# Performance work log

Hardware: AMD Instinct MI355X
Metric: run time of the kernel (lower is better)

Reference implementation:

```python
import jax, jax.numpy as jnp
import numpy as np

N_NODES = 50000
N_EDGES = 1600000
OUT_FEATURES = 32


def setup_inputs() -> dict:
    key = jax.random.key(0)
    k_edge, k_w = jax.random.split(key)
    edge = jax.random.randint(k_edge, (2, N_EDGES), 0, N_NODES, dtype=jnp.int64 if jax.config.jax_enable_x64 else jnp.int32)
    edge_w = jax.random.normal(k_w, (N_EDGES, OUT_FEATURES), dtype=jnp.float32)
    return {
        "edge": edge,
        "edge_w": edge_w,
        "num_nodes": N_NODES,
        "E": N_EDGES,
        "out_features": OUT_FEATURES,
    }


def reference(edge, edge_w, num_nodes, E, out_features):
    # torch: sparse_coo_tensor(edge, edge_w, [N, N, F]); torch.sparse.sum(dim=1).to_dense()
    # == segment-sum of edge_w over source indices edge[0] into N buckets.
    src = edge[0]  # (E,)
    out = jax.ops.segment_sum(edge_w, src, num_segments=num_nodes)  # (N, F)
    return out
```

## Files before the change

kernel.cpp:

```cpp
#include <hip/hip_runtime.h>


constexpr int F = 32;
constexpr int NPB = 64;
constexpr int CAP = 3072;
constexpr int SLOT = 97;
constexpr int TILE = 6272;
constexpr int TSLOT = 44;
constexpr int STH = 1024;
constexpr int ATH = 512;

__global__ void __launch_bounds__(1024) zero_cursor(int* __restrict__ cursor, int nbuck) {
  int t = threadIdx.x;
  if (t < nbuck) cursor[t] = 0;
}

__global__ void __launch_bounds__(STH) bucket_scatter(
    const int* __restrict__ src, int* __restrict__ cursor,
    int* __restrict__ blist, int E, int nbuck) {
  extern __shared__ int lds[];
  int* slots = lds;
  int* scnt  = lds + nbuck * TSLOT;
  int t0 = blockIdx.x * TILE;
  int mEnd = min(TILE, E - t0);
  if (mEnd <= 0) return;
  for (int i = threadIdx.x; i < nbuck; i += STH) scnt[i] = 0;
  __syncthreads();
  const int4* src4 = reinterpret_cast<const int4*>(src + t0);
  int m4 = mEnd >> 2;
  for (int j = threadIdx.x; j < m4; j += STH) {
    int4 v = src4[j];
    int e = t0 + (j << 2);
    int b0 = v.x >> 6, p0 = atomicAdd(&scnt[b0], 1);
    if (p0 < TSLOT) slots[b0 * TSLOT + p0] = ((v.x & 63) << 21) | e;
    int b1 = v.y >> 6, p1 = atomicAdd(&scnt[b1], 1);
    if (p1 < TSLOT) slots[b1 * TSLOT + p1] = ((v.y & 63) << 21) | (e + 1);
    int b2 = v.z >> 6, p2 = atomicAdd(&scnt[b2], 1);
    if (p2 < TSLOT) slots[b2 * TSLOT + p2] = ((v.z & 63) << 21) | (e + 2);
    int b3 = v.w >> 6, p3 = atomicAdd(&scnt[b3], 1);
    if (p3 < TSLOT) slots[b3 * TSLOT + p3] = ((v.w & 63) << 21) | (e + 3);
  }
  for (int j = (m4 << 2) + threadIdx.x; j < mEnd; j += STH) {
    int sv = src[t0 + j];
    int b = sv >> 6, p = atomicAdd(&scnt[b], 1);
    if (p < TSLOT) slots[b * TSLOT + p] = ((sv & 63) << 21) | (t0 + j);
  }
  __syncthreads();
  for (int b = threadIdx.x; b < nbuck; b += STH) {
    int c = min(scnt[b], TSLOT);
    if (c) {
      int gbase = b * CAP + atomicAdd(&cursor[b], c);
      const int* s = &slots[b * TSLOT];
      for (int j = 0; j < c; ++j) blist[gbase + j] = s[j];
    }
  }
}

__global__ void __launch_bounds__(ATH) bucket_accum(
    const int* __restrict__ blist, const int* __restrict__ cursor,
    const float* __restrict__ w, float* __restrict__ out, int N) {
  __shared__ int sorted[NPB * SLOT];
  __shared__ int cur[NPB];
  int b = blockIdx.x;
  int t = threadIdx.x;
  int g = t >> 3;
  int ln = t & 7;
  const float4* w4 = reinterpret_cast<const float4*>(w);

  if (t < NPB) cur[t] = 0;
  int beg = b * CAP;
  int cnt_b = cursor[b];
  __syncthreads();

  const int4* bl4 = reinterpret_cast<const int4*>(blist + beg);
  int m4 = cnt_b >> 2;
  for (int i = t; i < m4; i += ATH) {
    int4 v = bl4[i];
    int p0 = atomicAdd(&cur[v.x >> 21], 1);
    if (p0 < SLOT) sorted[(v.x >> 21) * SLOT + p0] = v.x & 0x1FFFFF;
    int p1 = atomicAdd(&cur[v.y >> 21], 1);
    if (p1 < SLOT) sorted[(v.y >> 21) * SLOT + p1] = v.y & 0x1FFFFF;
    int p2 = atomicAdd(&cur[v.z >> 21], 1);
    if (p2 < SLOT) sorted[(v.z >> 21) * SLOT + p2] = v.z & 0x1FFFFF;
    int p3 = atomicAdd(&cur[v.w >> 21], 1);
    if (p3 < SLOT) sorted[(v.w >> 21) * SLOT + p3] = v.w & 0x1FFFFF;
  }
  for (int i = (m4 << 2) + t; i < cnt_b; i += ATH) {
    int v = blist[beg + i];
    int node = v >> 21;
    int pos = atomicAdd(&cur[node], 1);
    if (pos < SLOT) sorted[node * SLOT + pos] = v & 0x1FFFFF;
  }
  __syncthreads();

  int ke = min(cur[g], SLOT);
  const int* myList = &sorted[g * SLOT];
  float4 a0{0,0,0,0}, a1{0,0,0,0}, a2{0,0,0,0}, a3{0,0,0,0},
         a4{0,0,0,0}, a5{0,0,0,0}, a6{0,0,0,0}, a7{0,0,0,0};
  int km = ke - 1;
  for (int k = 0; k < ke; k += 8) {
    int e0 = myList[min(k,     km)], e1 = myList[min(k + 1, km)];
    int e2 = myList[min(k + 2, km)], e3 = myList[min(k + 3, km)];
    int e4 = myList[min(k + 4, km)], e5 = myList[min(k + 5, km)];
    int e6 = myList[min(k + 6, km)], e7 = myList[min(k + 7, km)];
    float m1 = (k + 1 <= km) ? 1.f : 0.f, m2 = (k + 2 <= km) ? 1.f : 0.f;
    float m3 = (k + 3 <= km) ? 1.f : 0.f, m4f = (k + 4 <= km) ? 1.f : 0.f;
    float m5 = (k + 5 <= km) ? 1.f : 0.f, m6 = (k + 6 <= km) ? 1.f : 0.f;
    float m7 = (k + 7 <= km) ? 1.f : 0.f;
    float4 v0 = w4[(size_t)e0 * 8 + ln], v1 = w4[(size_t)e1 * 8 + ln];
    float4 v2 = w4[(size_t)e2 * 8 + ln], v3 = w4[(size_t)e3 * 8 + ln];
    float4 v4 = w4[(size_t)e4 * 8 + ln], v5 = w4[(size_t)e5 * 8 + ln];
    float4 v6 = w4[(size_t)e6 * 8 + ln], v7 = w4[(size_t)e7 * 8 + ln];
    a0.x += v0.x;      a0.y += v0.y;      a0.z += v0.z;      a0.w += v0.w;
    a1.x += m1 * v1.x; a1.y += m1 * v1.y; a1.z += m1 * v1.z; a1.w += m1 * v1.w;
    a2.x += m2 * v2.x; a2.y += m2 * v2.y; a2.z += m2 * v2.z; a2.w += m2 * v2.w;
    a3.x += m3 * v3.x; a3.y += m3 * v3.y; a3.z += m3 * v3.z; a3.w += m3 * v3.w;
    a4.x += m4f * v4.x; a4.y += m4f * v4.y; a4.z += m4f * v4.z; a4.w += m4f * v4.w;
    a5.x += m5 * v5.x; a5.y += m5 * v5.y; a5.z += m5 * v5.z; a5.w += m5 * v5.w;
    a6.x += m6 * v6.x; a6.y += m6 * v6.y; a6.z += m6 * v6.z; a6.w += m6 * v6.w;
    a7.x += m7 * v7.x; a7.y += m7 * v7.y; a7.z += m7 * v7.z; a7.w += m7 * v7.w;
  }
  a0.x += a1.x + a2.x + a3.x + a4.x + a5.x + a6.x + a7.x;
  a0.y += a1.y + a2.y + a3.y + a4.y + a5.y + a6.y + a7.y;
  a0.z += a1.z + a2.z + a3.z + a4.z + a5.z + a6.z + a7.z;
  a0.w += a1.w + a2.w + a3.w + a4.w + a5.w + a6.w + a7.w;
  int node = b * NPB + g;
  if (node < N)
    reinterpret_cast<float4*>(out)[(size_t)node * 8 + ln] = a0;
}

extern "C" void kernel_launch(void* const* d_in, const int* in_sizes, int n_in,
                              void* d_out, int out_size, void* d_ws, size_t ws_size,
                              hipStream_t stream) {
  const int* edge = (const int*)d_in[0];
  const float* edge_w = (const float*)d_in[1];
  const int E = in_sizes[0] / 2;
  const int* src = edge;
  float* out = (float*)d_out;
  const int N = out_size / F;
  const int nbuck = (N + NPB - 1) / NPB;

  int* ws = (int*)d_ws;
  int* cursor = ws;
  int* blist  = cursor + nbuck;

  size_t ldsBytes = (size_t)(nbuck * TSLOT + nbuck) * sizeof(int);

  zero_cursor<<<1, 1024, 0, stream>>>(cursor, nbuck);
  bucket_scatter<<<(E + TILE - 1) / TILE, STH, ldsBytes, stream>>>(src, cursor, blist, E, nbuck);
  bucket_accum<<<nbuck, ATH, 0, stream>>>(blist, cursor, edge_w, out, N);
}
```

Measured before the change: 62.87 us.

## Fuse zero, scatter and accumulate into one cooperative persistent kernel

Merges the three launches (cursor zeroing, bucket scatter, bucket accumulation) into a single cooperative kernel of 256 blocks separated by grid-wide syncs, with each 1024-thread block handling two buckets at a time in the accumulate phase. The goal is to remove launch gaps and inter-kernel drain between stages. The trade-off is grid.sync overhead, a grid fixed at 256 blocks with large LDS that may limit occupancy, and the scatter phase now assuming 256 tiles cover all edges, since E=1.6M needs 256 tiles of 6272.

```diff
diff --git a/kernel.cpp b/kernel.cpp
--- a/kernel.cpp
+++ b/kernel.cpp
@@ -1,5 +1,8 @@
 #include <hip/hip_runtime.h>
+#include <hip/hip_cooperative_groups.h>
 
+
+namespace cg = cooperative_groups;
 
 constexpr int F = 32;
 constexpr int NPB = 64;
@@ -7,126 +10,131 @@
 constexpr int SLOT = 97;
 constexpr int TILE = 6272;
 constexpr int TSLOT = 44;
-constexpr int STH = 1024;
-constexpr int ATH = 512;
+constexpr int FTH = 1024;
+constexpr int NBLK = 256;
 
-__global__ void __launch_bounds__(1024) zero_cursor(int* __restrict__ cursor, int nbuck) {
+__global__ void __launch_bounds__(FTH) fused_segsum(
+    const int* __restrict__ src, int* __restrict__ cursor,
+    int* __restrict__ blist, const float* __restrict__ w,
+    float* __restrict__ out, int E, int N, int nbuck) {
+  extern __shared__ int lds[];
+  cg::grid_group grid = cg::this_grid();
   int t = threadIdx.x;
-  if (t < nbuck) cursor[t] = 0;
-}
+  int gtid = blockIdx.x * FTH + t;
 
-__global__ void __launch_bounds__(STH) bucket_scatter(
-    const int* __restrict__ src, int* __restrict__ cursor,
-    int* __restrict__ blist, int E, int nbuck) {
-  extern __shared__ int lds[];
-  int* slots = lds;
-  int* scnt  = lds + nbuck * TSLOT;
-  int t0 = blockIdx.x * TILE;
-  int mEnd = min(TILE, E - t0);
-  if (mEnd <= 0) return;
-  for (int i = threadIdx.x; i < nbuck; i += STH) scnt[i] = 0;
-  __syncthreads();
-  const int4* src4 = reinterpret_cast<const int4*>(src + t0);
-  int m4 = mEnd >> 2;
-  for (int j = threadIdx.x; j < m4; j += STH) {
-    int4 v = src4[j];
-    int e = t0 + (j << 2);
-    int b0 = v.x >> 6, p0 = atomicAdd(&scnt[b0], 1);
-    if (p0 < TSLOT) slots[b0 * TSLOT + p0] = ((v.x & 63) << 21) | e;
-    int b1 = v.y >> 6, p1 = atomicAdd(&scnt[b1], 1);
-    if (p1 < TSLOT) slots[b1 * TSLOT + p1] = ((v.y & 63) << 21) | (e + 1);
-    int b2 = v.z >> 6, p2 = atomicAdd(&scnt[b2], 1);
-    if (p2 < TSLOT) slots[b2 * TSLOT + p2] = ((v.z & 63) << 21) | (e + 2);
-    int b3 = v.w >> 6, p3 = atomicAdd(&scnt[b3], 1);
-    if (p3 < TSLOT) slots[b3 * TSLOT + p3] = ((v.w & 63) << 21) | (e + 3);
-  }
-  for (int j = (m4 << 2) + threadIdx.x; j < mEnd; j += STH) {
-    int sv = src[t0 + j];
-    int b = sv >> 6, p = atomicAdd(&scnt[b], 1);
-    if (p < TSLOT) slots[b * TSLOT + p] = ((sv & 63) << 21) | (t0 + j);
-  }
-  __syncthreads();
-  for (int b = threadIdx.x; b < nbuck; b += STH) {
-    int c = min(scnt[b], TSLOT);
-    if (c) {
-      int gbase = b * CAP + atomicAdd(&cursor[b], c);
-      const int* s = &slots[b * TSLOT];
-      for (int j = 0; j < c; ++j) blist[gbase + j] = s[j];
+  if (gtid < nbuck) cursor[gtid] = 0;
+  grid.sync();
+
+  {
+    int* slots = lds;
+    int* scnt  = lds + nbuck * TSLOT;
+    int t0 = blockIdx.x * TILE;
+    int mEnd = min(TILE, E - t0);
+    for (int i = t; i < nbuck; i += FTH) scnt[i] = 0;
+    __syncthreads();
+    const int4* src4 = reinterpret_cast<const int4*>(src + t0);
+    int m4 = mEnd >> 2;
+    for (int j = t; j < m4; j += FTH) {
+      int4 v = src4[j];
+      int e = t0 + (j << 2);
+      int b0 = v.x >> 6, p0 = atomicAdd(&scnt[b0], 1);
+      if (p0 < TSLOT) slots[b0 * TSLOT + p0] = ((v.x & 63) << 21) | e;
+      int b1 = v.y >> 6, p1 = atomicAdd(&scnt[b1], 1);
+      if (p1 < TSLOT) slots[b1 * TSLOT + p1] = ((v.y & 63) << 21) | (e + 1);
+      int b2 = v.z >> 6, p2 = atomicAdd(&scnt[b2], 1);
+      if (p2 < TSLOT) slots[b2 * TSLOT + p2] = ((v.z & 63) << 21) | (e + 2);
+      int b3 = v.w >> 6, p3 = atomicAdd(&scnt[b3], 1);
+      if (p3 < TSLOT) slots[b3 * TSLOT + p3] = ((v.w & 63) << 21) | (e + 3);
+    }
+    for (int j = (m4 << 2) + t; j < mEnd; j += FTH) {
+      int sv = src[t0 + j];
+      int b = sv >> 6, p = atomicAdd(&scnt[b], 1);
+      if (p < TSLOT) slots[b * TSLOT + p] = ((sv & 63) << 21) | (t0 + j);
+    }
+    __syncthreads();
+    for (int b = t; b < nbuck; b += FTH) {
+      int c = min(scnt[b], TSLOT);
+      if (c) {
+        int gbase = b * CAP + atomicAdd(&cursor[b], c);
+        const int* s = &slots[b * TSLOT];
+        for (int j = 0; j < c; ++j) blist[gbase + j] = s[j];
+      }
     }
   }
-}
+  __threadfence();
+  grid.sync();
 
-__global__ void __launch_bounds__(ATH) bucket_accum(
-    const int* __restrict__ blist, const int* __restrict__ cursor,
-    const float* __restrict__ w, float* __restrict__ out, int N) {
-  __shared__ int sorted[NPB * SLOT];
-  __shared__ int cur[NPB];
-  int b = blockIdx.x;
-  int t = threadIdx.x;
-  int g = t >> 3;
-  int ln = t & 7;
-  const float4* w4 = reinterpret_cast<const float4*>(w);
+  {
+    int h = t >> 9;
+    int ht = t & 511;
+    int* hl = lds + h * (NPB * SLOT + NPB);
+    int* sorted = hl;
+    int* cur = hl + NPB * SLOT;
+    int g = ht >> 3;
+    int ln = ht & 7;
+    const float4* w4 = reinterpret_cast<const float4*>(w);
 
-  if (t < NPB) cur[t] = 0;
-  int beg = b * CAP;
-  int cnt_b = cursor[b];
-  __syncthreads();
-
-  const int4* bl4 = reinterpret_cast<const int4*>(blist + beg);
-  int m4 = cnt_b >> 2;
-  for (int i = t; i < m4; i += ATH) {
-    int4 v = bl4[i];
-    int p0 = atomicAdd(&cur[v.x >> 21], 1);
-    if (p0 < SLOT) sorted[(v.x >> 21) * SLOT + p0] = v.x & 0x1FFFFF;
-    int p1 = atomicAdd(&cur[v.y >> 21], 1);
-    if (p1 < SLOT) sorted[(v.y >> 21) * SLOT + p1] = v.y & 0x1FFFFF;
-    int p2 = atomicAdd(&cur[v.z >> 21], 1);
-    if (p2 < SLOT) sorted[(v.z >> 21) * SLOT + p2] = v.z & 0x1FFFFF;
-    int p3 = atomicAdd(&cur[v.w >> 21], 1);
-    if (p3 < SLOT) sorted[(v.w >> 21) * SLOT + p3] = v.w & 0x1FFFFF;
+    for (int b = blockIdx.x * 2 + h; b < nbuck; b += NBLK * 2) {
+      if (ht < NPB) cur[ht] = 0;
+      int beg = b * CAP;
+      __syncthreads();
+      int cnt_b = cursor[b];
+      const int4* bl4 = reinterpret_cast<const int4*>(blist + beg);
+      int m4 = cnt_b >> 2;
+      for (int i = ht; i < m4; i += 512) {
+        int4 v = bl4[i];
+        int p0 = atomicAdd(&cur[v.x >> 21], 1);
+        if (p0 < SLOT) sorted[(v.x >> 21) * SLOT + p0] = v.x & 0x1FFFFF;
+        int p1 = atomicAdd(&cur[v.y >> 21], 1);
+        if (p1 < SLOT) sorted[(v.y >> 21) * SLOT + p1] = v.y & 0x1FFFFF;
+        int p2 = atomicAdd(&cur[v.z >> 21], 1);
+        if (p2 < SLOT) sorted[(v.z >> 21) * SLOT + p2] = v.z & 0x1FFFFF;
+        int p3 = atomicAdd(&cur[v.w >> 21], 1);
+        if (p3 < SLOT) sorted[(v.w >> 21) * SLOT + p3] = v.w & 0x1FFFFF;
+      }
+      for (int i = (m4 << 2) + ht; i < cnt_b; i += 512) {
+        int v = blist[beg + i];
+        int node = v >> 21;
+        int pos = atomicAdd(&cur[node], 1);
+        if (pos < SLOT) sorted[node * SLOT + pos] = v & 0x1FFFFF;
+      }
+      __syncthreads();
+      int ke = min(cur[g], SLOT);
+      const int* myList = &sorted[g * SLOT];
+      float4 a0{0,0,0,0}, a1{0,0,0,0}, a2{0,0,0,0}, a3{0,0,0,0},
+             a4{0,0,0,0}, a5{0,0,0,0}, a6{0,0,0,0}, a7{0,0,0,0};
+      int km = ke - 1;
+      for (int k = 0; k < ke; k += 8) {
+        int e0 = myList[min(k,     km)], e1 = myList[min(k + 1, km)];
+        int e2 = myList[min(k + 2, km)], e3 = myList[min(k + 3, km)];
+        int e4 = myList[min(k + 4, km)], e5 = myList[min(k + 5, km)];
+        int e6 = myList[min(k + 6, km)], e7 = myList[min(k + 7, km)];
+        float m1 = (k + 1 <= km) ? 1.f : 0.f, m2 = (k + 2 <= km) ? 1.f : 0.f;
+        float m3 = (k + 3 <= km) ? 1.f : 0.f, m4f = (k + 4 <= km) ? 1.f : 0.f;
+        float m5 = (k + 5 <= km) ? 1.f : 0.f, m6 = (k + 6 <= km) ? 1.f : 0.f;
+        float m7 = (k + 7 <= km) ? 1.f : 0.f;
+        float4 v0 = w4[(size_t)e0 * 8 + ln], v1 = w4[(size_t)e1 * 8 + ln];
+        float4 v2 = w4[(size_t)e2 * 8 + ln], v3 = w4[(size_t)e3 * 8 + ln];
+        float4 v4 = w4[(size_t)e4 * 8 + ln], v5 = w4[(size_t)e5 * 8 + ln];
+        float4 v6 = w4[(size_t)e6 * 8 + ln], v7 = w4[(size_t)e7 * 8 + ln];
+        a0.x += v0.x;       a0.y += v0.y;       a0.z += v0.z;       a0.w += v0.w;
+        a1.x += m1 * v1.x;  a1.y += m1 * v1.y;  a1.z += m1 * v1.z;  a1.w += m1 * v1.w;
+        a2.x += m2 * v2.x;  a2.y += m2 * v2.y;  a2.z += m2 * v2.z;  a2.w += m2 * v2.w;
+        a3.x += m3 * v3.x;  a3.y += m3 * v3.y;  a3.z += m3 * v3.z;  a3.w += m3 * v3.w;
+        a4.x += m4f * v4.x; a4.y += m4f * v4.y; a4.z += m4f * v4.z; a4.w += m4f * v4.w;
+        a5.x += m5 * v5.x;  a5.y += m5 * v5.y;  a5.z += m5 * v5.z;  a5.w += m5 * v5.w;
+        a6.x += m6 * v6.x;  a6.y += m6 * v6.y;  a6.z += m6 * v6.z;  a6.w += m6 * v6.w;
+        a7.x += m7 * v7.x;  a7.y += m7 * v7.y;  a7.z += m7 * v7.z;  a7.w += m7 * v7.w;
+      }
+      a0.x += a1.x + a2.x + a3.x + a4.x + a5.x + a6.x + a7.x;
+      a0.y += a1.y + a2.y + a3.y + a4.y + a5.y + a6.y + a7.y;
+      a0.z += a1.z + a2.z + a3.z + a4.z + a5.z + a6.z + a7.z;
+      a0.w += a1.w + a2.w + a3.w + a4.w + a5.w + a6.w + a7.w;
+      int node = b * NPB + g;
+      if (node < N)
+        reinterpret_cast<float4*>(out)[(size_t)node * 8 + ln] = a0;
+    }
   }
-  for (int i = (m4 << 2) + t; i < cnt_b; i += ATH) {
-    int v = blist[beg + i];
-    int node = v >> 21;
-    int pos = atomicAdd(&cur[node], 1);
-    if (pos < SLOT) sorted[node * SLOT + pos] = v & 0x1FFFFF;
-  }
-  __syncthreads();
-
-  int ke = min(cur[g], SLOT);
-  const int* myList = &sorted[g * SLOT];
-  float4 a0{0,0,0,0}, a1{0,0,0,0}, a2{0,0,0,0}, a3{0,0,0,0},
-         a4{0,0,0,0}, a5{0,0,0,0}, a6{0,0,0,0}, a7{0,0,0,0};
-  int km = ke - 1;
-  for (int k = 0; k < ke; k += 8) {
-    int e0 = myList[min(k,     km)], e1 = myList[min(k + 1, km)];
-    int e2 = myList[min(k + 2, km)], e3 = myList[min(k + 3, km)];
-    int e4 = myList[min(k + 4, km)], e5 = myList[min(k + 5, km)];
-    int e6 = myList[min(k + 6, km)], e7 = myList[min(k + 7, km)];
-    float m1 = (k + 1 <= km) ? 1.f : 0.f, m2 = (k + 2 <= km) ? 1.f : 0.f;
-    float m3 = (k + 3 <= km) ? 1.f : 0.f, m4f = (k + 4 <= km) ? 1.f : 0.f;
-    float m5 = (k + 5 <= km) ? 1.f : 0.f, m6 = (k + 6 <= km) ? 1.f : 0.f;
-    float m7 = (k + 7 <= km) ? 1.f : 0.f;
-    float4 v0 = w4[(size_t)e0 * 8 + ln], v1 = w4[(size_t)e1 * 8 + ln];
-    float4 v2 = w4[(size_t)e2 * 8 + ln], v3 = w4[(size_t)e3 * 8 + ln];
-    float4 v4 = w4[(size_t)e4 * 8 + ln], v5 = w4[(size_t)e5 * 8 + ln];
-    float4 v6 = w4[(size_t)e6 * 8 + ln], v7 = w4[(size_t)e7 * 8 + ln];
-    a0.x += v0.x;      a0.y += v0.y;      a0.z += v0.z;      a0.w += v0.w;
-    a1.x += m1 * v1.x; a1.y += m1 * v1.y; a1.z += m1 * v1.z; a1.w += m1 * v1.w;
-    a2.x += m2 * v2.x; a2.y += m2 * v2.y; a2.z += m2 * v2.z; a2.w += m2 * v2.w;
-    a3.x += m3 * v3.x; a3.y += m3 * v3.y; a3.z += m3 * v3.z; a3.w += m3 * v3.w;
-    a4.x += m4f * v4.x; a4.y += m4f * v4.y; a4.z += m4f * v4.z; a4.w += m4f * v4.w;
-    a5.x += m5 * v5.x; a5.y += m5 * v5.y; a5.z += m5 * v5.z; a5.w += m5 * v5.w;
-    a6.x += m6 * v6.x; a6.y += m6 * v6.y; a6.z += m6 * v6.z; a6.w += m6 * v6.w;
-    a7.x += m7 * v7.x; a7.y += m7 * v7.y; a7.z += m7 * v7.z; a7.w += m7 * v7.w;
-  }
-  a0.x += a1.x + a2.x + a3.x + a4.x + a5.x + a6.x + a7.x;
-  a0.y += a1.y + a2.y + a3.y + a4.y + a5.y + a6.y + a7.y;
-  a0.z += a1.z + a2.z + a3.z + a4.z + a5.z + a6.z + a7.z;
-  a0.w += a1.w + a2.w + a3.w + a4.w + a5.w + a6.w + a7.w;
-  int node = b * NPB + g;
-  if (node < N)
-    reinterpret_cast<float4*>(out)[(size_t)node * 8 + ln] = a0;
 }
 
 extern "C" void kernel_launch(void* const* d_in, const int* in_sizes, int n_in,
@@ -134,19 +142,22 @@
                               hipStream_t stream) {
   const int* edge = (const int*)d_in[0];
   const float* edge_w = (const float*)d_in[1];
-  const int E = in_sizes[0] / 2;
+  int E = in_sizes[0] / 2;
   const int* src = edge;
   float* out = (float*)d_out;
-  const int N = out_size / F;
-  const int nbuck = (N + NPB - 1) / NPB;
+  int N = out_size / F;
+  int nbuck = (N + NPB - 1) / NPB;
 
   int* ws = (int*)d_ws;
   int* cursor = ws;
   int* blist  = cursor + nbuck;
 
-  size_t ldsBytes = (size_t)(nbuck * TSLOT + nbuck) * sizeof(int);
+  size_t ldsB = (size_t)(nbuck * (TSLOT + 1)) * sizeof(int);
+  size_t ldsC = (size_t)(2 * (NPB * SLOT + NPB)) * sizeof(int);
+  size_t ldsBytes = ldsB > ldsC ? ldsB : ldsC;
 
-  zero_cursor<<<1, 1024, 0, stream>>>(cursor, nbuck);
-  bucket_scatter<<<(E + TILE - 1) / TILE, STH, ldsBytes, stream>>>(src, cursor, blist, E, nbuck);
-  bucket_accum<<<nbuck, ATH, 0, stream>>>(blist, cursor, edge_w, out, N);
+  void* args[] = {(void*)&src, (void*)&cursor, (void*)&blist,
+                  (void*)&edge_w, (void*)&out, (void*)&E, (void*)&N, (void*)&nbuck};
+  hipLaunchCooperativeKernel(reinterpret_cast<void*>(fused_segsum),
+                             dim3(NBLK), dim3(FTH), args, ldsBytes, stream);
 }
```

Result: slower. 228.0 us (+262.6%).
